# Optimization experiments

Hardware: AMD Instinct MI355X
Metric: run time of the kernel (lower is better)

The kernel has to match this reference:

```python
import math
import jax, jax.numpy as jnp
import numpy as np

B, N = 1, 512
C_S, C_Z, C_H, H, PQ, PV = 384, 128, 16, 12, 4, 8
CONCAT = H * C_Z + H * C_H + H * PV * 3 + H * PV  # 2112
W_C = math.sqrt(2.0 / (9.0 * PQ))
W_L = math.sqrt(1.0 / 3.0)


def setup_inputs() -> dict:
    key = jax.random.key(0)
    ks = jax.random.split(key, 16)
    sc = 0.02
    return {
        "s": jax.random.normal(ks[0], (B, N, C_S), jnp.float32),
        "z": jax.random.normal(ks[1], (B, N, N, C_Z), jnp.float32),
        "R": jax.random.normal(ks[2], (B, N, 3, 3), jnp.float32),
        "t": jax.random.normal(ks[3], (B, N, 3), jnp.float32),
        "mask": jnp.ones((B, N), dtype=bool),
        "Wqkv": jax.random.normal(ks[4], (C_S, 3 * H * C_H), jnp.float32) * sc,
        "Wqk_pts": jax.random.normal(ks[5], (C_S, 2 * H * PQ * 3), jnp.float32) * sc,
        "bqk_pts": jnp.zeros((2 * H * PQ * 3,), jnp.float32),
        "Wv_pts": jax.random.normal(ks[6], (C_S, H * PV * 3), jnp.float32) * sc,
        "bv_pts": jnp.zeros((H * PV * 3,), jnp.float32),
        "Wb": jax.random.normal(ks[7], (C_Z, H), jnp.float32) * sc,
        "bb": jnp.zeros((H,), jnp.float32),
        "gamma": jnp.full((H,), 0.541324854612918, jnp.float32),
        "Wfin": jax.random.normal(ks[8], (CONCAT, C_S), jnp.float32) * sc,
        "bfin": jnp.zeros((C_S,), jnp.float32),
    }


def _apply_rigid(R, t, pts):
    # R: [B,N,3,3], t: [B,N,3], pts: [B,N,H,P,3] -> global frame
    return jnp.einsum('bnxy,bnhpy->bnhpx', R, pts) + t[:, :, None, None, :]


def _invert_apply_rigid(R, t, pts):
    # R^T (pts - t)
    return jnp.einsum('bnyx,bnhpy->bnhpx', R, pts - t[:, :, None, None, :])


def reference(s, z, R, t, mask, Wqkv, Wqk_pts, bqk_pts, Wv_pts, bv_pts,
              Wb, bb, gamma, Wfin, bfin):
    b_, n_ = s.shape[0], s.shape[1]
    qkv = (s @ Wqkv).reshape(b_, n_, 3, H, C_H)
    q, k, v = qkv[:, :, 0], qkv[:, :, 1], qkv[:, :, 2]
    term1 = jnp.einsum('bihc,bjhc->bhij', q, k) / math.sqrt(C_H)
    term2 = jnp.transpose(z @ Wb + bb, (0, 3, 1, 2))  # [B,H,i,j]

    qk_pts = (s @ Wqk_pts + bqk_pts).reshape(b_, n_, 2, H, PQ, 3)
    q_pts, k_pts = qk_pts[:, :, 0], qk_pts[:, :, 1]
    qg = _apply_rigid(R, t, q_pts)  # [B,N,H,PQ,3]
    kg = _apply_rigid(R, t, k_pts)
    # squared distance summed over points and xyz -> [B,i,j,H]
    diff2 = jnp.sum((qg[:, :, None] - kg[:, None]) ** 2, axis=(-2, -1))
    term3 = (jax.nn.softplus(gamma)[None, :, None, None] * (W_C / 2.0)
             * jnp.transpose(diff2, (0, 3, 1, 2)))

    logits = W_L * (term1 + term2 - term3)
    logits = jnp.where(mask[:, None, None, :], logits, -1e9)
    aw = jax.nn.softmax(logits, axis=-1)  # [B,H,i,j]

    out_tilde = jnp.einsum('bhij,bijc->bihc', aw, z)
    out = jnp.einsum('bhij,bjhc->bihc', aw, v)

    v_pts = (s @ Wv_pts + bv_pts).reshape(b_, n_, H, PV, 3)
    vg = _apply_rigid(R, t, v_pts)
    o_global = jnp.einsum('bhij,bjhvx->bihvx', aw, vg)
    o_vec = _invert_apply_rigid(R, t, o_global)  # [B,N,H,PV,3]
    o_norm = jnp.sqrt(jnp.sum(o_vec ** 2, axis=-1) + 1e-8)

    feats = jnp.concatenate([
        out_tilde.reshape(b_, n_, -1),
        out.reshape(b_, n_, -1),
        o_vec.reshape(b_, n_, -1),
        o_norm.reshape(b_, n_, -1),
    ], axis=-1)
    return feats @ Wfin + bfin
```

## Files before the change

### kernel.cpp

```cpp
#include <hip/hip_runtime.h>
#include <math.h>

#define NSEQ 512
#define CS   384
#define NH   12
#define CHD  16
#define CZ   128
#define CONCATD 2112

#define W_L      0.57735026918962576f
#define W_C_HALF 0.117851130197757925f

typedef float f32x4 __attribute__((ext_vector_type(4)));
typedef short bf16x8 __attribute__((ext_vector_type(8)));
typedef unsigned int u32x2 __attribute__((ext_vector_type(2)));
typedef unsigned int u32x4 __attribute__((ext_vector_type(4)));

__device__ __forceinline__ unsigned short f2bf(float f) {
    union { float f; unsigned int u; } v; v.f = f;
    unsigned int u = v.u + 0x7FFFu + ((v.u >> 16) & 1u);
    return (unsigned short)(u >> 16);
}
__device__ __forceinline__ float bf2f(unsigned short u) {
    union { unsigned int i; float f; } v; v.i = ((unsigned int)u) << 16; return v.f;
}

#define MFMA16(A, B, C) __builtin_amdgcn_mfma_f32_16x16x32_bf16((A), (B), (C), 0, 0, 0)

#define RAWBAR() do {                                          \
    __builtin_amdgcn_sched_barrier(0);                         \
    asm volatile("s_waitcnt lgkmcnt(0)" ::: "memory");         \
    __builtin_amdgcn_s_barrier();                              \
    __builtin_amdgcn_sched_barrier(0);                         \
} while (0)

__global__ __launch_bounds__(256) void ipa_prep(
    const float* __restrict__ s, const float* __restrict__ Wqkv,
    const float* __restrict__ Wqk, const float* __restrict__ Wv,
    const float* __restrict__ bqk, const float* __restrict__ bv,
    const float* __restrict__ Wfin,
    unsigned short* __restrict__ sb, unsigned short* __restrict__ WcatT,
    float* __restrict__ biasv, unsigned short* __restrict__ WfinT)
{
    __shared__ float tile[32][33];
    if (blockIdx.x >= 314) {
        int b = blockIdx.x - 314;
        int kt = b / 12, nt = b - kt * 12;
        int k0 = kt * 32, n0 = nt * 32;
        #pragma unroll
        for (int it = 0; it < 4; ++it) {
            int idx = it * 256 + threadIdx.x;
            int ty = idx >> 5, tx = idx & 31;
            tile[ty][tx] = Wfin[(size_t)(k0 + ty) * 384 + n0 + tx];
        }
        __syncthreads();
        #pragma unroll
        for (int it = 0; it < 4; ++it) {
            int idx = it * 256 + threadIdx.x;
            int ty = idx >> 5, tx = idx & 31;
            WfinT[(size_t)(n0 + ty) * 2112 + k0 + tx] = f2bf(tile[tx][ty]);
        }
        return;
    }
    int v = blockIdx.x * 256 + threadIdx.x;
    if (v < 24576) {
        const float* src = s + (size_t)v * 8;
        f32x4 a = *(const f32x4*)src, b = *(const f32x4*)(src + 4);
        u32x4 pk;
        pk[0] = (unsigned)f2bf(a[0]) | ((unsigned)f2bf(a[1]) << 16);
        pk[1] = (unsigned)f2bf(a[2]) | ((unsigned)f2bf(a[3]) << 16);
        pk[2] = (unsigned)f2bf(b[0]) | ((unsigned)f2bf(b[1]) << 16);
        pk[3] = (unsigned)f2bf(b[2]) | ((unsigned)f2bf(b[3]) << 16);
        *(u32x4*)(sb + (size_t)v * 8) = pk;
    } else if (v < 79872) {
        int v2 = v - 24576;
        int n = v2 / 48;
        int kq = (v2 - n * 48) * 8;
        const float* W; int stride; int col; float sc = 1.f;
        if (n < 576)      { W = Wqkv; stride = 576; col = n;       if (n < 192) sc = 0.25f; }
        else if (n < 864) { W = Wqk;  stride = 288; col = n - 576; }
        else              { W = Wv;   stride = 288; col = n - 864; }
        const float* src = W + (size_t)kq * stride + col;
        unsigned int pk[4];
        #pragma unroll
        for (int e = 0; e < 4; ++e) {
            float v0 = src[(size_t)(2 * e) * stride] * sc;
            float v1 = src[(size_t)(2 * e + 1) * stride] * sc;
            pk[e] = (unsigned)f2bf(v0) | ((unsigned)f2bf(v1) << 16);
        }
        u32x4 pkv = {pk[0], pk[1], pk[2], pk[3]};
        *(u32x4*)(WcatT + (size_t)n * 384 + kq) = pkv;
    } else if (v < 80160) {
        int c0 = (v - 79872) * 4;
        #pragma unroll
        for (int e = 0; e < 4; ++e) {
            int c = c0 + e;
            biasv[c] = (c < 576) ? 0.f : ((c < 864) ? bqk[c - 576] : bv[c - 864]);
        }
    }
}

__global__ __launch_bounds__(128) void ipa_projgemm(
    const unsigned short* __restrict__ sb, const unsigned short* __restrict__ WcatT,
    const float* __restrict__ biasv, float* __restrict__ proj)
{
    const int n0 = blockIdx.x * 64, m0 = blockIdx.y * 32;
    const int tid = threadIdx.x, lane = tid & 63, wv = tid >> 6;
    __shared__ __align__(16) unsigned short A_l[32][136];
    __shared__ __align__(16) unsigned short B_l[64][136];
    f32x4 C[4];
    const f32x4 ZV = {0.f, 0.f, 0.f, 0.f};
    #pragma unroll
    for (int nf = 0; nf < 4; ++nf) C[nf] = ZV;

    #pragma unroll
    for (int kc = 0; kc < 3; ++kc) {
        const int k0 = kc * 128;
        __syncthreads();
        #pragma unroll
        for (int it = 0; it < 4; ++it) {
            int v = it * 128 + tid;
            int row = v >> 4, c8 = v & 15;
            *(u32x4*)&A_l[row][c8 * 8] =
                *(const u32x4*)(sb + (size_t)(m0 + row) * 384 + k0 + c8 * 8);
        }
        #pragma unroll
        for (int it = 0; it < 8; ++it) {
            int v = it * 128 + tid;
            int row = v >> 4, c8 = v & 15;
            *(u32x4*)&B_l[row][c8 * 8] =
                *(const u32x4*)(WcatT + (size_t)(n0 + row) * 384 + k0 + c8 * 8);
        }
        __syncthreads();
        const int koff = (lane >> 4) * 8;
        #pragma unroll
        for (int ks = 0; ks < 4; ++ks) {
            bf16x8 Af = *(const bf16x8*)&A_l[wv * 16 + (lane & 15)][ks * 32 + koff];
            #pragma unroll
            for (int nf = 0; nf < 4; ++nf) {
                bf16x8 Bf = *(const bf16x8*)&B_l[nf * 16 + (lane & 15)][ks * 32 + koff];
                C[nf] = MFMA16(Af, Bf, C[nf]);
            }
        }
    }
    #pragma unroll
    for (int nf = 0; nf < 4; ++nf) {
        int col = n0 + nf * 16 + (lane & 15);
        float bval = biasv[col];
        #pragma unroll
        for (int r = 0; r < 4; ++r) {
            int row = m0 + wv * 16 + (lane >> 4) * 4 + r;
            proj[(size_t)row * 1152 + col] = C[nf][r] + bval;
        }
    }
}

__global__ __launch_bounds__(256) void ipa_projep(
    const float* __restrict__ proj, const float* __restrict__ R, const float* __restrict__ t,
    const float* __restrict__ gamma,
    unsigned short* __restrict__ Aaug, unsigned short* __restrict__ Baug,
    unsigned short* __restrict__ VcatT, float* __restrict__ rq, float* __restrict__ rk)
{
    const int half = threadIdx.x >> 7;
    const int i = blockIdx.x * 2 + half;
    const int st = threadIdx.x & 127;
    __shared__ float R_l[2][9], t_l[2][3], sq_l[2][96];
    __shared__ float sh_l[12];

    if (st < 9) R_l[half][st] = R[i * 9 + st];
    if (st >= 12 && st < 15) t_l[half][st - 12] = t[i * 3 + st - 12];
    if (threadIdx.x >= 240 && threadIdx.x < 252) {
        int h = threadIdx.x - 240;
        float spg = logf(1.f + __expf(gamma[h])) * W_C_HALF;
        sh_l[h] = sqrtf(2.f * spg);
    }
    __syncthreads();

    const float* row = proj + (size_t)i * 1152;

    for (int c = st; c < 576; c += 128) {
        unsigned short b16 = f2bf(row[c]);
        if (c < 192) {
            Aaug[((size_t)(c >> 4) * 512 + i) * 32 + (c & 15)] = b16;
        } else if (c < 384) {
            int cc = c - 192;
            Baug[((size_t)(cc >> 4) * 512 + i) * 32 + (cc & 15)] = b16;
        } else {
            int cc = c - 384;
            VcatT[((size_t)((cc >> 4) * 48 + (cc & 15))) * 512 + i] = b16;
        }
    }

    const float* Rr = R_l[half];
    const float* tt = t_l[half];
    for (int pt = st; pt < 192; pt += 128) {
        if (pt < 96) {
            int lp = (pt < 48) ? pt : pt - 48;
            int h = lp >> 2, p = lp & 3;
            int base = 576 + pt * 3;
            float p0 = row[base], p1 = row[base + 1], p2 = row[base + 2];
            float sh = sh_l[h];
            float g0 = (Rr[0] * p0 + Rr[1] * p1 + Rr[2] * p2 + tt[0]) * sh;
            float g1 = (Rr[3] * p0 + Rr[4] * p1 + Rr[5] * p2 + tt[1]) * sh;
            float g2 = (Rr[6] * p0 + Rr[7] * p1 + Rr[8] * p2 + tt[2]) * sh;
            sq_l[half][pt] = g0 * g0 + g1 * g1 + g2 * g2;
            unsigned short* dst =
                (pt < 48 ? Aaug : Baug) + ((size_t)h * 512 + i) * 32 + 16 + p * 3;
            dst[0] = f2bf(g0); dst[1] = f2bf(g1); dst[2] = f2bf(g2);
        } else {
            int vp = pt - 96;
            int h = vp >> 3, vv = vp & 7;
            int base = 864 + vp * 3;
            float p0 = row[base], p1 = row[base + 1], p2 = row[base + 2];
            float g0 = Rr[0] * p0 + Rr[1] * p1 + Rr[2] * p2 + tt[0];
            float g1 = Rr[3] * p0 + Rr[4] * p1 + Rr[5] * p2 + tt[1];
            float g2 = Rr[6] * p0 + Rr[7] * p1 + Rr[8] * p2 + tt[2];
            size_t rbase = ((size_t)h * 48 + 16 + vv * 3) * 512 + i;
            VcatT[rbase] = f2bf(g0);
            VcatT[rbase + 512] = f2bf(g1);
            VcatT[rbase + 1024] = f2bf(g2);
        }
    }
    __syncthreads();

    if (st < 24) {
        int qk = st / 12, h = st - qk * 12;
        int b0 = qk * 48 + h * 4;
        float ssum = sq_l[half][b0] + sq_l[half][b0 + 1]
                   + sq_l[half][b0 + 2] + sq_l[half][b0 + 3];
        (qk ? rk : rq)[h * 512 + i] = 0.5f * ssum;
    }
    if (st >= 32 && st < 56) {
        int e = st - 32;
        int mt = e / 12, h = e - mt * 12;
        *(unsigned long long*)((mt ? Baug : Aaug) + ((size_t)h * 512 + i) * 32 + 28) = 0ull;
    }
}

__global__ __launch_bounds__(256) void ipa_term2n(
    const float* __restrict__ z, const float* __restrict__ Wb, const float* __restrict__ bb,
    unsigned short* __restrict__ S)
{
    const int i = blockIdx.x >> 3;
    const int j0 = (blockIdx.x & 7) * 64;
    const int tid = threadIdx.x, lane = tid & 63, wv = tid >> 6;
    const int l15 = lane & 15, hi = lane >> 4;
    const int koff = hi * 8;
    __shared__ __align__(16) unsigned short z_l[64][136];

    bf16x8 wbf[4];
    #pragma unroll
    for (int ks = 0; ks < 4; ++ks) {
        bf16x8 rfr;
        #pragma unroll
        for (int e = 0; e < 8; ++e) {
            int c = ks * 32 + koff + e;
            float w = (l15 < 12) ? Wb[c * 12 + l15] : 0.f;
            rfr[e] = (short)f2bf(w);
        }
        wbf[ks] = rfr;
    }
    float bbv[4];
    #pragma unroll
    for (int r = 0; r < 4; ++r) { int h = hi * 4 + r; bbv[r] = (h < 12) ? bb[h] : 0.f; }

    #pragma unroll
    for (int it = 0; it < 4; ++it) {
        int u = it * 256 + tid;
        int row = u >> 4, c8 = u & 15;
        const float* src = z + ((size_t)(i * 512 + j0 + row)) * 128 + c8 * 8;
        f32x4 a = *(const f32x4*)src, b = *(const f32x4*)(src + 4);
        u32x4 pk;
        pk[0] = (unsigned)f2bf(a[0]) | ((unsigned)f2bf(a[1]) << 16);
        pk[1] = (unsigned)f2bf(a[2]) | ((unsigned)f2bf(a[3]) << 16);
        pk[2] = (unsigned)f2bf(b[0]) | ((unsigned)f2bf(b[1]) << 16);
        pk[3] = (unsigned)f2bf(b[2]) | ((unsigned)f2bf(b[3]) << 16);
        *(u32x4*)&z_l[row][c8 * 8] = pk;
    }
    __syncthreads();

    const int jcol = wv * 16 + l15;
    f32x4 C = {0.f, 0.f, 0.f, 0.f};
    #pragma unroll
    for (int ks = 0; ks < 4; ++ks)
        C = MFMA16(wbf[ks], *(const bf16x8*)&z_l[jcol][ks * 32 + koff], C);
    #pragma unroll
    for (int r = 0; r < 4; ++r) {
        int h = hi * 4 + r;
        if (h < 12)
            S[(size_t)h * 262144 + (size_t)i * 512 + j0 + jcol] = f2bf(C[r] + bbv[r]);
    }
}

__global__ __launch_bounds__(256) void ipa_smax(
    const unsigned short* __restrict__ S, const unsigned short* __restrict__ Aaug,
    const unsigned short* __restrict__ Baug, const float* __restrict__ rq,
    const float* __restrict__ rk, unsigned short* __restrict__ P1, float* __restrict__ l1)
{
    const int h = blockIdx.x, i0 = blockIdx.y * 16;
    const int tid = threadIdx.x, lane = tid & 63, wv = tid >> 6;
    const int col = lane & 15, hi = lane >> 4;
    __shared__ __align__(16) unsigned short Baug_l[512][40];
    __shared__ __align__(16) unsigned short Aaug_l[16][40];
    __shared__ float rk_l[512], rq_l[16];
    __shared__ float pmx[4][16], psm[4][16];

    for (int u = tid; u < 2048; u += 256) {
        int row = u >> 2, seg = u & 3;
        *(u32x4*)&Baug_l[row][seg * 8] =
            *(const u32x4*)(Baug + ((size_t)h * 512 + row) * 32 + seg * 8);
    }
    if (tid < 64) {
        int row = tid >> 2, seg = tid & 3;
        *(u32x4*)&Aaug_l[row][seg * 8] =
            *(const u32x4*)(Aaug + ((size_t)h * 512 + i0 + row) * 32 + seg * 8);
    }
    for (int u = tid; u < 512; u += 256) rk_l[u] = rk[h * 512 + u];
    if (tid >= 64 && tid < 80) rq_l[tid - 64] = rq[h * 512 + i0 + tid - 64];
    __syncthreads();

    const f32x4 ZV = {0.f, 0.f, 0.f, 0.f};
    bf16x8 Af = *(const bf16x8*)&Aaug_l[col][hi * 8];
    f32x4 C[8];
    #pragma unroll
    for (int nf = 0; nf < 8; ++nf) {
        int n = wv * 8 + nf;
        bf16x8 Bf = *(const bf16x8*)&Baug_l[n * 16 + col][hi * 8];
        C[nf] = MFMA16(Af, Bf, ZV);
    }
    const unsigned short* Srow = S + (size_t)h * 262144 + (size_t)i0 * 512;
    float rmax[4] = {-1e30f, -1e30f, -1e30f, -1e30f};
    #pragma unroll
    for (int nf = 0; nf < 8; ++nf) {
        int j = wv * 128 + nf * 16 + col;
        float rkj = rk_l[j];
        #pragma unroll
        for (int r = 0; r < 4; ++r) {
            int il = hi * 4 + r;
            float Sv = bf2f(Srow[(size_t)il * 512 + j]);
            float L = W_L * (C[nf][r] + Sv - rq_l[il] - rkj);
            C[nf][r] = L;
            rmax[r] = fmaxf(rmax[r], L);
        }
    }
    #pragma unroll
    for (int o = 8; o; o >>= 1)
        #pragma unroll
        for (int r = 0; r < 4; ++r) rmax[r] = fmaxf(rmax[r], __shfl_xor(rmax[r], o));
    if (col == 0)
        #pragma unroll
        for (int r = 0; r < 4; ++r) pmx[wv][hi * 4 + r] = rmax[r];
    __syncthreads();
    float M[4], lsum[4] = {0.f, 0.f, 0.f, 0.f};
    #pragma unroll
    for (int r = 0; r < 4; ++r) {
        int il = hi * 4 + r;
        M[r] = fmaxf(fmaxf(pmx[0][il], pmx[1][il]), fmaxf(pmx[2][il], pmx[3][il]));
    }
    #pragma unroll
    for (int nf = 0; nf < 8; ++nf)
        #pragma unroll
        for (int r = 0; r < 4; ++r) {
            float p = __expf(C[nf][r] - M[r]);
            C[nf][r] = p;
            lsum[r] += p;
        }
    #pragma unroll
    for (int o = 8; o; o >>= 1)
        #pragma unroll
        for (int r = 0; r < 4; ++r) lsum[r] += __shfl_xor(lsum[r], o);
    if (col == 0)
        #pragma unroll
        for (int r = 0; r < 4; ++r) psm[wv][hi * 4 + r] = lsum[r];
    __syncthreads();
    if (wv == 0 && col == 0) {
        #pragma unroll
        for (int r = 0; r < 4; ++r) {
            int il = hi * 4 + r;
            l1[h * 512 + i0 + il] = psm[0][il] + psm[1][il] + psm[2][il] + psm[3][il];
        }
    }
    unsigned short* Prow = P1 + (size_t)h * 262144 + (size_t)i0 * 512;
    #pragma unroll
    for (int nf = 0; nf < 8; ++nf) {
        int j = wv * 128 + nf * 16 + col;
        #pragma unroll
        for (int r = 0; r < 4; ++r)
            Prow[(size_t)(hi * 4 + r) * 512 + j] = f2bf(C[nf][r]);
    }
}

__global__ __launch_bounds__(256) void ipa_ot2(
    const float* __restrict__ z, const unsigned short* __restrict__ P1,
    const float* __restrict__ l1, unsigned short* __restrict__ featsb)
{
    const int bid = blockIdx.x;
    const int i = bid >> 1;
    const int chalf = (bid & 1) * 64;
    const int tid = threadIdx.x, lane = tid & 63, wv = tid >> 6;
    const int l15 = lane & 15, hi = lane >> 4;
    const int koff = hi * 8;
    __shared__ __align__(16) unsigned short P_l[16][520];
    __shared__ __align__(16) unsigned short zT[2][64][72];

    for (int u = tid; u < 1024; u += 256) {
        int row = u >> 6, c8 = u & 63;
        *(u32x4*)&P_l[row][c8 * 8] =
            *(const u32x4*)(P1 + (size_t)row * 262144 + (size_t)i * 512 + c8 * 8);
    }
    __syncthreads();

    f32x4 sa[4];
    #pragma unroll
    for (int it = 0; it < 4; ++it) {
        int u = it * 256 + tid;
        int jj = u >> 4, c4l = u & 15;
        sa[it] = *(const f32x4*)(z + ((size_t)(i * 512 + jj)) * 128 + chalf + c4l * 4);
    }

    const f32x4 ZV = {0.f, 0.f, 0.f, 0.f};
    f32x4 Co = ZV;

    for (int jt = 0; jt < 8; ++jt) {
        const int cur = jt & 1;
        #pragma unroll
        for (int it = 0; it < 4; ++it) {
            int u = it * 256 + tid;
            int jj = u >> 4, c4l = u & 15;
            f32x4 zv = sa[it];
            unsigned short b0 = f2bf(zv[0]), b1 = f2bf(zv[1]), b2 = f2bf(zv[2]), b3 = f2bf(zv[3]);
            unsigned int w01 = (unsigned)b0 | ((unsigned)b1 << 16);
            unsigned int w23 = (unsigned)b2 | ((unsigned)b3 << 16);
            unsigned int p01 = (unsigned int)__shfl_xor((int)w01, 16);
            unsigned int p23 = (unsigned int)__shfl_xor((int)w23, 16);
            bool even = ((tid & 16) == 0);
            unsigned short q0 = (unsigned short)(p01 & 0xffff), q1 = (unsigned short)(p01 >> 16);
            unsigned short q2 = (unsigned short)(p23 & 0xffff), q3 = (unsigned short)(p23 >> 16);
            unsigned int w0, w1, w2, w3;
            if (even) {
                w0 = (unsigned)b0 | ((unsigned)q0 << 16); w1 = (unsigned)b1 | ((unsigned)q1 << 16);
                w2 = (unsigned)b2 | ((unsigned)q2 << 16); w3 = (unsigned)b3 | ((unsigned)q3 << 16);
            } else {
                w0 = (unsigned)q0 | ((unsigned)b0 << 16); w1 = (unsigned)q1 | ((unsigned)b1 << 16);
                w2 = (unsigned)q2 | ((unsigned)b2 << 16); w3 = (unsigned)q3 | ((unsigned)b3 << 16);
            }
            int jp = jj >> 1;
            int rot = ((c4l >> 1) & 3) + (even ? 0 : 2);
            #pragma unroll
            for (int ss = 0; ss < 2; ++ss) {
                int rr = (rot + ss) & 3;
                unsigned int val = (rr == 0) ? w0 : ((rr == 1) ? w1 : ((rr == 2) ? w2 : w3));
                *(unsigned int*)&zT[cur][4 * c4l + rr][2 * jp] = val;
            }
        }
        if (jt < 7) {
            const int j0n = (jt + 1) * 64;
            #pragma unroll
            for (int it = 0; it < 4; ++it) {
                int u = it * 256 + tid;
                int jj = u >> 4, c4l = u & 15;
                sa[it] = *(const f32x4*)(z + ((size_t)(i * 512 + j0n + jj)) * 128 + chalf + c4l * 4);
            }
        }
        RAWBAR();
        #pragma unroll
        for (int ks2 = 0; ks2 < 2; ++ks2) {
            bf16x8 Af = *(const bf16x8*)&P_l[l15][jt * 64 + ks2 * 32 + koff];
            bf16x8 Bf = *(const bf16x8*)&zT[cur][wv * 16 + l15][ks2 * 32 + koff];
            Co = MFMA16(Af, Bf, Co);
        }
    }

    #pragma unroll
    for (int r = 0; r < 4; ++r) {
        int h = hi * 4 + r;
        if (h < 12)
            featsb[(size_t)i * CONCATD + h * 128 + chalf + wv * 16 + l15]
                = f2bf(Co[r] / l1[h * 512 + i]);
    }
}

__global__ __launch_bounds__(256) void ipa_pv(
    const unsigned short* __restrict__ P1, const unsigned short* __restrict__ VcatT,
    const float* __restrict__ l1, const float* __restrict__ R,
    const float* __restrict__ t, unsigned short* __restrict__ featsb)
{
    const int h = blockIdx.x, i0 = blockIdx.y * 64;
    const int tid = threadIdx.x, lane = tid & 63, wv = tid >> 6;
    const int col = lane & 15, hi = lane >> 4;
    __shared__ __align__(16) unsigned short V_l[48][520];
    __shared__ float ogl[64][26];

    for (int u = tid; u < 3072; u += 256) {
        int row = u >> 6, c8 = u & 63;
        *(u32x4*)&V_l[row][c8 * 8] =
            *(const u32x4*)(VcatT + ((size_t)h * 48 + row) * 512 + c8 * 8);
    }
    __syncthreads();
    f32x4 C0 = {0.f,0.f,0.f,0.f}, C1 = C0, C2 = C0;
    const unsigned short* Pbase =
        P1 + (size_t)h * 262144 + (size_t)(i0 + wv * 16 + col) * 512;
    #pragma unroll
    for (int ks = 0; ks < 16; ++ks) {
        bf16x8 Af = *(const bf16x8*)(Pbase + ks * 32 + hi * 8);
        C0 = MFMA16(Af, *(const bf16x8*)&V_l[col][ks * 32 + hi * 8],      C0);
        C1 = MFMA16(Af, *(const bf16x8*)&V_l[16 + col][ks * 32 + hi * 8], C1);
        C2 = MFMA16(Af, *(const bf16x8*)&V_l[32 + col][ks * 32 + hi * 8], C2);
    }
    #pragma unroll
    for (int r = 0; r < 4; ++r) {
        int il = wv * 16 + hi * 4 + r;
        int irow = i0 + il;
        float inv = 1.f / l1[h * 512 + irow];
        featsb[(size_t)irow * CONCATD + 1536 + h * 16 + col] = f2bf(C0[r] * inv);
        ogl[il][col] = C1[r] * inv;
        if (col < 8) ogl[il][16 + col] = C2[r] * inv;
    }
    __syncthreads();

    #pragma unroll
    for (int it = 0; it < 2; ++it) {
        int item = it * 256 + tid;
        int il = item >> 3, v = item & 7;
        int i = i0 + il;
        const float* Rr = R + i * 9;
        const float* tt = t + i * 3;
        float g0 = ogl[il][v * 3 + 0] - tt[0];
        float g1 = ogl[il][v * 3 + 1] - tt[1];
        float g2 = ogl[il][v * 3 + 2] - tt[2];
        float o0 = Rr[0] * g0 + Rr[3] * g1 + Rr[6] * g2;
        float o1 = Rr[1] * g0 + Rr[4] * g1 + Rr[7] * g2;
        float o2 = Rr[2] * g0 + Rr[5] * g1 + Rr[8] * g2;
        unsigned short* frow = featsb + (size_t)i * CONCATD;
        frow[1728 + h * 24 + v * 3 + 0] = f2bf(o0);
        frow[1728 + h * 24 + v * 3 + 1] = f2bf(o1);
        frow[1728 + h * 24 + v * 3 + 2] = f2bf(o2);
        frow[2016 + h * 8 + v] = f2bf(sqrtf(o0 * o0 + o1 * o1 + o2 * o2 + 1e-8f));
    }
}

__global__ __launch_bounds__(128) void ipa_finalb(
    const unsigned short* __restrict__ featsb, const unsigned short* __restrict__ WfinT,
    float* __restrict__ fpart)
{
    const int n0 = blockIdx.x * 64, m0 = blockIdx.y * 32;
    const int k0 = blockIdx.z * 192;
    const int tid = threadIdx.x, lane = tid & 63, wv = tid >> 6;
    const int l15 = lane & 15, hi = lane >> 4;
    __shared__ __align__(16) unsigned short A_l[32][200];
    __shared__ __align__(16) unsigned short B_l[64][200];

    #pragma unroll
    for (int it = 0; it < 6; ++it) {
        int v = it * 128 + tid;
        int row = v / 24, c8 = v % 24;
        *(u32x4*)&A_l[row][c8 * 8] =
            *(const u32x4*)(featsb + (size_t)(m0 + row) * CONCATD + k0 + c8 * 8);
    }
    #pragma unroll
    for (int it = 0; it < 12; ++it) {
        int v = it * 128 + tid;
        int row = v / 24, c8 = v % 24;
        *(u32x4*)&B_l[row][c8 * 8] =
            *(const u32x4*)(WfinT + (size_t)(n0 + row) * 2112 + k0 + c8 * 8);
    }
    __syncthreads();

    const f32x4 ZV = {0.f, 0.f, 0.f, 0.f};
    f32x4 C[4];
    #pragma unroll
    for (int nf = 0; nf < 4; ++nf) C[nf] = ZV;
    const int koff = hi * 8;
    #pragma unroll
    for (int ks = 0; ks < 6; ++ks) {
        bf16x8 Af = *(const bf16x8*)&A_l[wv * 16 + l15][ks * 32 + koff];
        #pragma unroll
        for (int nf = 0; nf < 4; ++nf) {
            bf16x8 Bf = *(const bf16x8*)&B_l[nf * 16 + l15][ks * 32 + koff];
            C[nf] = MFMA16(Af, Bf, C[nf]);
        }
    }
    float* P = fpart + (size_t)blockIdx.z * (NSEQ * CS);
    #pragma unroll
    for (int nf = 0; nf < 4; ++nf) {
        int colx = n0 + nf * 16 + l15;
        #pragma unroll
        for (int r = 0; r < 4; ++r) {
            int row = m0 + wv * 16 + hi * 4 + r;
            P[(size_t)row * CS + colx] = C[nf][r];
        }
    }
}

__global__ __launch_bounds__(256) void ipa_reduceb(
    const float* __restrict__ fpart, const float* __restrict__ bias, float* __restrict__ out)
{
    int idx = blockIdx.x * 256 + threadIdx.x;
    f32x4 acc = ((const f32x4*)bias)[idx % (CS / 4)];
    #pragma unroll
    for (int kc = 0; kc < 11; ++kc)
        acc += ((const f32x4*)(fpart + (size_t)kc * (NSEQ * CS)))[idx];
    ((f32x4*)out)[idx] = acc;
}

extern "C" void kernel_launch(void* const* d_in, const int* in_sizes, int n_in,
                              void* d_out, int out_size, void* d_ws, size_t ws_size,
                              hipStream_t stream) {
    (void)in_sizes; (void)n_in; (void)out_size; (void)ws_size;
    const float* s    = (const float*)d_in[0];
    const float* z    = (const float*)d_in[1];
    const float* R    = (const float*)d_in[2];
    const float* t    = (const float*)d_in[3];
    const float* Wqkv = (const float*)d_in[5];
    const float* Wqk  = (const float*)d_in[6];
    const float* bqk  = (const float*)d_in[7];
    const float* Wv   = (const float*)d_in[8];
    const float* bv   = (const float*)d_in[9];
    const float* Wb   = (const float*)d_in[10];
    const float* bb   = (const float*)d_in[11];
    const float* gam  = (const float*)d_in[12];
    const float* Wfin = (const float*)d_in[13];
    const float* bfin = (const float*)d_in[14];
    float* out = (float*)d_out;

    char* w8 = (char*)d_ws;
    unsigned short* S     = (unsigned short*)(w8 + 0);
    unsigned short* P1    = (unsigned short*)(w8 + 6291456);
    unsigned short* featsb= (unsigned short*)(w8 + 12582912);
    unsigned short* WfinT = (unsigned short*)(w8 + 14745600);
    unsigned short* Aaug  = (unsigned short*)(w8 + 16908288);
    unsigned short* Baug  = (unsigned short*)(w8 + 17301504);
    unsigned short* VcatT = (unsigned short*)(w8 + 17694720);
    float* rq             = (float*)(w8 + 18284544);
    float* rk             = (float*)(w8 + 18309120);
    float* l1             = (float*)(w8 + 18333696);
    float* fpart          = (float*)(w8 + 0);
    float* proj           = (float*)(w8 + 0);
    unsigned short* sb    = (unsigned short*)(w8 + 2359296);
    unsigned short* WcatT = (unsigned short*)(w8 + 2752512);
    float* biasv          = (float*)(w8 + 3637248);

    ipa_prep<<<1106, 256, 0, stream>>>(s, Wqkv, Wqk, Wv, bqk, bv, Wfin,
                                       sb, WcatT, biasv, WfinT);
    ipa_projgemm<<<dim3(18, 16), 128, 0, stream>>>(sb, WcatT, biasv, proj);
    ipa_projep<<<256, 256, 0, stream>>>(proj, R, t, gam, Aaug, Baug, VcatT, rq, rk);
    ipa_term2n<<<4096, 256, 0, stream>>>(z, Wb, bb, S);
    ipa_smax<<<dim3(12, 32), 256, 0, stream>>>(S, Aaug, Baug, rq, rk, P1, l1);
    ipa_ot2<<<1024, 256, 0, stream>>>(z, P1, l1, featsb);
    ipa_pv<<<dim3(12, 8), 256, 0, stream>>>(P1, VcatT, l1, R, t, featsb);
    ipa_finalb<<<dim3(6, 16, 11), 128, 0, stream>>>(featsb, WfinT, fpart);
    ipa_reduceb<<<192, 256, 0, stream>>>(fpart, bfin, out);
}
```

Measured before the change: 93.33 us.

## Merge independent kernels into heterogeneous launches to cut launch count

Combines the projection GEMM with the z·Wb pair-bias kernel into one launch that branches on block index, and combines the out_tilde and point-value attention kernels likewise. Workspace buffers are relocated so the merged kernels do not overwrite each other's data. The intent is to remove launch gaps and let small, low-occupancy kernels overlap with larger ones. In exchange, the projection blocks leave half their warps idle, the PV path now stages V in two halves, and shared-memory sizing is set by the larger branch.

```diff
diff --git a/kernel.cpp b/kernel.cpp
--- a/kernel.cpp
+++ b/kernel.cpp
@@ -100,57 +100,117 @@
     }
 }
 
-__global__ __launch_bounds__(128) void ipa_projgemm(
+__global__ __launch_bounds__(256) void ipa_pg_t2(
     const unsigned short* __restrict__ sb, const unsigned short* __restrict__ WcatT,
-    const float* __restrict__ biasv, float* __restrict__ proj)
+    const float* __restrict__ biasv, float* __restrict__ proj,
+    const float* __restrict__ z, const float* __restrict__ Wb,
+    const float* __restrict__ bb, unsigned short* __restrict__ S)
 {
-    const int n0 = blockIdx.x * 64, m0 = blockIdx.y * 32;
+    __shared__ __align__(16) char smem[26112];
     const int tid = threadIdx.x, lane = tid & 63, wv = tid >> 6;
-    __shared__ __align__(16) unsigned short A_l[32][136];
-    __shared__ __align__(16) unsigned short B_l[64][136];
-    f32x4 C[4];
+    const int l15 = lane & 15, hi = lane >> 4;
+    const int koff = hi * 8;
     const f32x4 ZV = {0.f, 0.f, 0.f, 0.f};
-    #pragma unroll
-    for (int nf = 0; nf < 4; ++nf) C[nf] = ZV;
-
-    #pragma unroll
-    for (int kc = 0; kc < 3; ++kc) {
-        const int k0 = kc * 128;
-        __syncthreads();
-        #pragma unroll
-        for (int it = 0; it < 4; ++it) {
-            int v = it * 128 + tid;
-            int row = v >> 4, c8 = v & 15;
-            *(u32x4*)&A_l[row][c8 * 8] =
-                *(const u32x4*)(sb + (size_t)(m0 + row) * 384 + k0 + c8 * 8);
-        }
-        #pragma unroll
-        for (int it = 0; it < 8; ++it) {
-            int v = it * 128 + tid;
-            int row = v >> 4, c8 = v & 15;
-            *(u32x4*)&B_l[row][c8 * 8] =
-                *(const u32x4*)(WcatT + (size_t)(n0 + row) * 384 + k0 + c8 * 8);
-        }
-        __syncthreads();
-        const int koff = (lane >> 4) * 8;
-        #pragma unroll
-        for (int ks = 0; ks < 4; ++ks) {
-            bf16x8 Af = *(const bf16x8*)&A_l[wv * 16 + (lane & 15)][ks * 32 + koff];
+
+    if (blockIdx.x < 288) {
+        const int n0 = ((int)blockIdx.x % 18) * 64;
+        const int m0 = ((int)blockIdx.x / 18) * 32;
+        unsigned short (*A_l)[136] = (unsigned short(*)[136])smem;
+        unsigned short (*B_l)[136] = (unsigned short(*)[136])(smem + 8704);
+        f32x4 C[4];
+        #pragma unroll
+        for (int nf = 0; nf < 4; ++nf) C[nf] = ZV;
+
+        #pragma unroll
+        for (int kc = 0; kc < 3; ++kc) {
+            const int k0 = kc * 128;
+            __syncthreads();
+            #pragma unroll
+            for (int it = 0; it < 2; ++it) {
+                int v = it * 256 + tid;
+                int row = v >> 4, c8 = v & 15;
+                *(u32x4*)&A_l[row][c8 * 8] =
+                    *(const u32x4*)(sb + (size_t)(m0 + row) * 384 + k0 + c8 * 8);
+            }
+            #pragma unroll
+            for (int it = 0; it < 4; ++it) {
+                int v = it * 256 + tid;
+                int row = v >> 4, c8 = v & 15;
+                *(u32x4*)&B_l[row][c8 * 8] =
+                    *(const u32x4*)(WcatT + (size_t)(n0 + row) * 384 + k0 + c8 * 8);
+            }
+            __syncthreads();
+            if (wv < 2) {
+                #pragma unroll
+                for (int ks = 0; ks < 4; ++ks) {
+                    bf16x8 Af = *(const bf16x8*)&A_l[wv * 16 + l15][ks * 32 + koff];
+                    #pragma unroll
+                    for (int nf = 0; nf < 4; ++nf) {
+                        bf16x8 Bf = *(const bf16x8*)&B_l[nf * 16 + l15][ks * 32 + koff];
+                        C[nf] = MFMA16(Af, Bf, C[nf]);
+                    }
+                }
+            }
+        }
+        if (wv < 2) {
             #pragma unroll
             for (int nf = 0; nf < 4; ++nf) {
-                bf16x8 Bf = *(const bf16x8*)&B_l[nf * 16 + (lane & 15)][ks * 32 + koff];
-                C[nf] = MFMA16(Af, Bf, C[nf]);
-            }
-        }
-    }
-    #pragma unroll
-    for (int nf = 0; nf < 4; ++nf) {
-        int col = n0 + nf * 16 + (lane & 15);
-        float bval = biasv[col];
+                int col = n0 + nf * 16 + l15;
+                float bval = biasv[col];
+                #pragma unroll
+                for (int r = 0; r < 4; ++r) {
+                    int row = m0 + wv * 16 + hi * 4 + r;
+                    proj[(size_t)row * 1152 + col] = C[nf][r] + bval;
+                }
+            }
+        }
+    } else {
+        const int b = blockIdx.x - 288;
+        const int i = b >> 3;
+        const int j0 = (b & 7) * 64;
+        unsigned short (*z_l)[136] = (unsigned short(*)[136])smem;
+
+        bf16x8 wbf[4];
+        #pragma unroll
+        for (int ks = 0; ks < 4; ++ks) {
+            bf16x8 rfr;
+            #pragma unroll
+            for (int e = 0; e < 8; ++e) {
+                int c = ks * 32 + koff + e;
+                float w = (l15 < 12) ? Wb[c * 12 + l15] : 0.f;
+                rfr[e] = (short)f2bf(w);
+            }
+            wbf[ks] = rfr;
+        }
+        float bbv[4];
+        #pragma unroll
+        for (int r = 0; r < 4; ++r) { int h = hi * 4 + r; bbv[r] = (h < 12) ? bb[h] : 0.f; }
+
+        #pragma unroll
+        for (int it = 0; it < 4; ++it) {
+            int u = it * 256 + tid;
+            int row = u >> 4, c8 = u & 15;
+            const float* src = z + ((size_t)(i * 512 + j0 + row)) * 128 + c8 * 8;
+            f32x4 a = *(const f32x4*)src, bq = *(const f32x4*)(src + 4);
+            u32x4 pk;
+            pk[0] = (unsigned)f2bf(a[0]) | ((unsigned)f2bf(a[1]) << 16);
+            pk[1] = (unsigned)f2bf(a[2]) | ((unsigned)f2bf(a[3]) << 16);
+            pk[2] = (unsigned)f2bf(bq[0]) | ((unsigned)f2bf(bq[1]) << 16);
+            pk[3] = (unsigned)f2bf(bq[2]) | ((unsigned)f2bf(bq[3]) << 16);
+            *(u32x4*)&z_l[row][c8 * 8] = pk;
+        }
+        __syncthreads();
+
+        const int jcol = wv * 16 + l15;
+        f32x4 C = ZV;
+        #pragma unroll
+        for (int ks = 0; ks < 4; ++ks)
+            C = MFMA16(wbf[ks], *(const bf16x8*)&z_l[jcol][ks * 32 + koff], C);
         #pragma unroll
         for (int r = 0; r < 4; ++r) {
-            int row = m0 + wv * 16 + (lane >> 4) * 4 + r;
-            proj[(size_t)row * 1152 + col] = C[nf][r] + bval;
+            int h = hi * 4 + r;
+            if (h < 12)
+                S[(size_t)h * 262144 + (size_t)i * 512 + j0 + jcol] = f2bf(C[r] + bbv[r]);
         }
     }
 }
@@ -237,61 +297,6 @@
     }
 }
 
-__global__ __launch_bounds__(256) void ipa_term2n(
-    const float* __restrict__ z, const float* __restrict__ Wb, const float* __restrict__ bb,
-    unsigned short* __restrict__ S)
-{
-    const int i = blockIdx.x >> 3;
-    const int j0 = (blockIdx.x & 7) * 64;
-    const int tid = threadIdx.x, lane = tid & 63, wv = tid >> 6;
-    const int l15 = lane & 15, hi = lane >> 4;
-    const int koff = hi * 8;
-    __shared__ __align__(16) unsigned short z_l[64][136];
-
-    bf16x8 wbf[4];
-    #pragma unroll
-    for (int ks = 0; ks < 4; ++ks) {
-        bf16x8 rfr;
-        #pragma unroll
-        for (int e = 0; e < 8; ++e) {
-            int c = ks * 32 + koff + e;
-            float w = (l15 < 12) ? Wb[c * 12 + l15] : 0.f;
-            rfr[e] = (short)f2bf(w);
-        }
-        wbf[ks] = rfr;
-    }
-    float bbv[4];
-    #pragma unroll
-    for (int r = 0; r < 4; ++r) { int h = hi * 4 + r; bbv[r] = (h < 12) ? bb[h] : 0.f; }
-
-    #pragma unroll
-    for (int it = 0; it < 4; ++it) {
-        int u = it * 256 + tid;
-        int row = u >> 4, c8 = u & 15;
-        const float* src = z + ((size_t)(i * 512 + j0 + row)) * 128 + c8 * 8;
-        f32x4 a = *(const f32x4*)src, b = *(const f32x4*)(src + 4);
-        u32x4 pk;
-        pk[0] = (unsigned)f2bf(a[0]) | ((unsigned)f2bf(a[1]) << 16);
-        pk[1] = (unsigned)f2bf(a[2]) | ((unsigned)f2bf(a[3]) << 16);
-        pk[2] = (unsigned)f2bf(b[0]) | ((unsigned)f2bf(b[1]) << 16);
-        pk[3] = (unsigned)f2bf(b[2]) | ((unsigned)f2bf(b[3]) << 16);
-        *(u32x4*)&z_l[row][c8 * 8] = pk;
-    }
-    __syncthreads();
-
-    const int jcol = wv * 16 + l15;
-    f32x4 C = {0.f, 0.f, 0.f, 0.f};
-    #pragma unroll
-    for (int ks = 0; ks < 4; ++ks)
-        C = MFMA16(wbf[ks], *(const bf16x8*)&z_l[jcol][ks * 32 + koff], C);
-    #pragma unroll
-    for (int r = 0; r < 4; ++r) {
-        int h = hi * 4 + r;
-        if (h < 12)
-            S[(size_t)h * 262144 + (size_t)i * 512 + j0 + jcol] = f2bf(C[r] + bbv[r]);
-    }
-}
-
 __global__ __launch_bounds__(256) void ipa_smax(
     const unsigned short* __restrict__ S, const unsigned short* __restrict__ Aaug,
     const unsigned short* __restrict__ Baug, const float* __restrict__ rq,
@@ -390,152 +395,155 @@
     }
 }
 
-__global__ __launch_bounds__(256) void ipa_ot2(
+__global__ __launch_bounds__(256) void ipa_otpv(
     const float* __restrict__ z, const unsigned short* __restrict__ P1,
-    const float* __restrict__ l1, unsigned short* __restrict__ featsb)
+    const float* __restrict__ l1, const unsigned short* __restrict__ VcatT,
+    const float* __restrict__ R, const float* __restrict__ t,
+    unsigned short* __restrict__ featsb)
 {
-    const int bid = blockIdx.x;
-    const int i = bid >> 1;
-    const int chalf = (bid & 1) * 64;
+    __shared__ __align__(16) char smem[35072];
     const int tid = threadIdx.x, lane = tid & 63, wv = tid >> 6;
     const int l15 = lane & 15, hi = lane >> 4;
     const int koff = hi * 8;
-    __shared__ __align__(16) unsigned short P_l[16][520];
-    __shared__ __align__(16) unsigned short zT[2][64][72];
-
-    for (int u = tid; u < 1024; u += 256) {
-        int row = u >> 6, c8 = u & 63;
-        *(u32x4*)&P_l[row][c8 * 8] =
-            *(const u32x4*)(P1 + (size_t)row * 262144 + (size_t)i * 512 + c8 * 8);
-    }
-    __syncthreads();
-
-    f32x4 sa[4];
-    #pragma unroll
-    for (int it = 0; it < 4; ++it) {
-        int u = it * 256 + tid;
-        int jj = u >> 4, c4l = u & 15;
-        sa[it] = *(const f32x4*)(z + ((size_t)(i * 512 + jj)) * 128 + chalf + c4l * 4);
-    }
-
     const f32x4 ZV = {0.f, 0.f, 0.f, 0.f};
-    f32x4 Co = ZV;
-
-    for (int jt = 0; jt < 8; ++jt) {
-        const int cur = jt & 1;
+
+    if (blockIdx.x < 1024) {
+        const int i = blockIdx.x >> 1;
+        const int chalf = ((int)blockIdx.x & 1) * 64;
+        unsigned short (*P_l)[520] = (unsigned short(*)[520])smem;
+        typedef unsigned short zt_t[64][72];
+        zt_t* zT = (zt_t*)(smem + 16640);
+
+        for (int u = tid; u < 1024; u += 256) {
+            int row = u >> 6, c8 = u & 63;
+            *(u32x4*)&P_l[row][c8 * 8] =
+                *(const u32x4*)(P1 + (size_t)row * 262144 + (size_t)i * 512 + c8 * 8);
+        }
+        __syncthreads();
+
+        f32x4 sa[4];
         #pragma unroll
         for (int it = 0; it < 4; ++it) {
             int u = it * 256 + tid;
             int jj = u >> 4, c4l = u & 15;
-            f32x4 zv = sa[it];
-            unsigned short b0 = f2bf(zv[0]), b1 = f2bf(zv[1]), b2 = f2bf(zv[2]), b3 = f2bf(zv[3]);
-            unsigned int w01 = (unsigned)b0 | ((unsigned)b1 << 16);
-            unsigned int w23 = (unsigned)b2 | ((unsigned)b3 << 16);
-            unsigned int p01 = (unsigned int)__shfl_xor((int)w01, 16);
-            unsigned int p23 = (unsigned int)__shfl_xor((int)w23, 16);
-            bool even = ((tid & 16) == 0);
-            unsigned short q0 = (unsigned short)(p01 & 0xffff), q1 = (unsigned short)(p01 >> 16);
-            unsigned short q2 = (unsigned short)(p23 & 0xffff), q3 = (unsigned short)(p23 >> 16);
-            unsigned int w0, w1, w2, w3;
-            if (even) {
-                w0 = (unsigned)b0 | ((unsigned)q0 << 16); w1 = (unsigned)b1 | ((unsigned)q1 << 16);
-                w2 = (unsigned)b2 | ((unsigned)q2 << 16); w3 = (unsigned)b3 | ((unsigned)q3 << 16);
-            } else {
-                w0 = (unsigned)q0 | ((unsigned)b0 << 16); w1 = (unsigned)q1 | ((unsigned)b1 << 16);
-                w2 = (unsigned)q2 | ((unsigned)b2 << 16); w3 = (unsigned)q3 | ((unsigned)b3 << 16);
-            }
-            int jp = jj >> 1;
-            int rot = ((c4l >> 1) & 3) + (even ? 0 : 2);
-            #pragma unroll
-            for (int ss = 0; ss < 2; ++ss) {
-                int rr = (rot + ss) & 3;
-                unsigned int val = (rr == 0) ? w0 : ((rr == 1) ? w1 : ((rr == 2) ? w2 : w3));
-                *(unsigned int*)&zT[cur][4 * c4l + rr][2 * jp] = val;
-            }
-        }
-        if (jt < 7) {
-            const int j0n = (jt + 1) * 64;
+            sa[it] = *(const f32x4*)(z + ((size_t)(i * 512 + jj)) * 128 + chalf + c4l * 4);
+        }
+
+        f32x4 Co = ZV;
+        for (int jt = 0; jt < 8; ++jt) {
+            const int cur = jt & 1;
             #pragma unroll
             for (int it = 0; it < 4; ++it) {
                 int u = it * 256 + tid;
                 int jj = u >> 4, c4l = u & 15;
-                sa[it] = *(const f32x4*)(z + ((size_t)(i * 512 + j0n + jj)) * 128 + chalf + c4l * 4);
-            }
-        }
-        RAWBAR();
-        #pragma unroll
-        for (int ks2 = 0; ks2 < 2; ++ks2) {
-            bf16x8 Af = *(const bf16x8*)&P_l[l15][jt * 64 + ks2 * 32 + koff];
-            bf16x8 Bf = *(const bf16x8*)&zT[cur][wv * 16 + l15][ks2 * 32 + koff];
-            Co = MFMA16(Af, Bf, Co);
-        }
-    }
-
-    #pragma unroll
-    for (int r = 0; r < 4; ++r) {
-        int h = hi * 4 + r;
-        if (h < 12)
-            featsb[(size_t)i * CONCATD + h * 128 + chalf + wv * 16 + l15]
-                = f2bf(Co[r] / l1[h * 512 + i]);
-    }
-}
-
-__global__ __launch_bounds__(256) void ipa_pv(
-    const unsigned short* __restrict__ P1, const unsigned short* __restrict__ VcatT,
-    const float* __restrict__ l1, const float* __restrict__ R,
-    const float* __restrict__ t, unsigned short* __restrict__ featsb)
-{
-    const int h = blockIdx.x, i0 = blockIdx.y * 64;
-    const int tid = threadIdx.x, lane = tid & 63, wv = tid >> 6;
-    const int col = lane & 15, hi = lane >> 4;
-    __shared__ __align__(16) unsigned short V_l[48][520];
-    __shared__ float ogl[64][26];
-
-    for (int u = tid; u < 3072; u += 256) {
-        int row = u >> 6, c8 = u & 63;
-        *(u32x4*)&V_l[row][c8 * 8] =
-            *(const u32x4*)(VcatT + ((size_t)h * 48 + row) * 512 + c8 * 8);
-    }
-    __syncthreads();
-    f32x4 C0 = {0.f,0.f,0.f,0.f}, C1 = C0, C2 = C0;
-    const unsigned short* Pbase =
-        P1 + (size_t)h * 262144 + (size_t)(i0 + wv * 16 + col) * 512;
-    #pragma unroll
-    for (int ks = 0; ks < 16; ++ks) {
-        bf16x8 Af = *(const bf16x8*)(Pbase + ks * 32 + hi * 8);
-        C0 = MFMA16(Af, *(const bf16x8*)&V_l[col][ks * 32 + hi * 8],      C0);
-        C1 = MFMA16(Af, *(const bf16x8*)&V_l[16 + col][ks * 32 + hi * 8], C1);
-        C2 = MFMA16(Af, *(const bf16x8*)&V_l[32 + col][ks * 32 + hi * 8], C2);
-    }
-    #pragma unroll
-    for (int r = 0; r < 4; ++r) {
-        int il = wv * 16 + hi * 4 + r;
-        int irow = i0 + il;
-        float inv = 1.f / l1[h * 512 + irow];
-        featsb[(size_t)irow * CONCATD + 1536 + h * 16 + col] = f2bf(C0[r] * inv);
-        ogl[il][col] = C1[r] * inv;
-        if (col < 8) ogl[il][16 + col] = C2[r] * inv;
-    }
-    __syncthreads();
-
-    #pragma unroll
-    for (int it = 0; it < 2; ++it) {
-        int item = it * 256 + tid;
-        int il = item >> 3, v = item & 7;
-        int i = i0 + il;
-        const float* Rr = R + i * 9;
-        const float* tt = t + i * 3;
-        float g0 = ogl[il][v * 3 + 0] - tt[0];
-        float g1 = ogl[il][v * 3 + 1] - tt[1];
-        float g2 = ogl[il][v * 3 + 2] - tt[2];
-        float o0 = Rr[0] * g0 + Rr[3] * g1 + Rr[6] * g2;
-        float o1 = Rr[1] * g0 + Rr[4] * g1 + Rr[7] * g2;
-        float o2 = Rr[2] * g0 + Rr[5] * g1 + Rr[8] * g2;
-        unsigned short* frow = featsb + (size_t)i * CONCATD;
-        frow[1728 + h * 24 + v * 3 + 0] = f2bf(o0);
-        frow[1728 + h * 24 + v * 3 + 1] = f2bf(o1);
-        frow[1728 + h * 24 + v * 3 + 2] = f2bf(o2);
-        frow[2016 + h * 8 + v] = f2bf(sqrtf(o0 * o0 + o1 * o1 + o2 * o2 + 1e-8f));
+                f32x4 zv = sa[it];
+                unsigned short b0 = f2bf(zv[0]), b1 = f2bf(zv[1]), b2 = f2bf(zv[2]), b3 = f2bf(zv[3]);
+                unsigned int w01 = (unsigned)b0 | ((unsigned)b1 << 16);
+                unsigned int w23 = (unsigned)b2 | ((unsigned)b3 << 16);
+                unsigned int p01 = (unsigned int)__shfl_xor((int)w01, 16);
+                unsigned int p23 = (unsigned int)__shfl_xor((int)w23, 16);
+                bool even = ((tid & 16) == 0);
+                unsigned short q0 = (unsigned short)(p01 & 0xffff), q1 = (unsigned short)(p01 >> 16);
+                unsigned short q2 = (unsigned short)(p23 & 0xffff), q3 = (unsigned short)(p23 >> 16);
+                unsigned int w0, w1, w2, w3;
+                if (even) {
+                    w0 = (unsigned)b0 | ((unsigned)q0 << 16); w1 = (unsigned)b1 | ((unsigned)q1 << 16);
+                    w2 = (unsigned)b2 | ((unsigned)q2 << 16); w3 = (unsigned)b3 | ((unsigned)q3 << 16);
+                } else {
+                    w0 = (unsigned)q0 | ((unsigned)b0 << 16); w1 = (unsigned)q1 | ((unsigned)b1 << 16);
+                    w2 = (unsigned)q2 | ((unsigned)b2 << 16); w3 = (unsigned)q3 | ((unsigned)b3 << 16);
+                }
+                int jp = jj >> 1;
+                int rot = ((c4l >> 1) & 3) + (even ? 0 : 2);
+                #pragma unroll
+                for (int ss = 0; ss < 2; ++ss) {
+                    int rr = (rot + ss) & 3;
+                    unsigned int val = (rr == 0) ? w0 : ((rr == 1) ? w1 : ((rr == 2) ? w2 : w3));
+                    *(unsigned int*)&zT[cur][4 * c4l + rr][2 * jp] = val;
+                }
+            }
+            if (jt < 7) {
+                const int j0n = (jt + 1) * 64;
+                #pragma unroll
+                for (int it = 0; it < 4; ++it) {
+                    int u = it * 256 + tid;
+                    int jj = u >> 4, c4l = u & 15;
+                    sa[it] = *(const f32x4*)(z + ((size_t)(i * 512 + j0n + jj)) * 128 + chalf + c4l * 4);
+                }
+            }
+            RAWBAR();
+            #pragma unroll
+            for (int ks2 = 0; ks2 < 2; ++ks2) {
+                bf16x8 Af = *(const bf16x8*)&P_l[l15][jt * 64 + ks2 * 32 + koff];
+                bf16x8 Bf = *(const bf16x8*)&zT[cur][wv * 16 + l15][ks2 * 32 + koff];
+                Co = MFMA16(Af, Bf, Co);
+            }
+        }
+
+        #pragma unroll
+        for (int r = 0; r < 4; ++r) {
+            int h = hi * 4 + r;
+            if (h < 12)
+                featsb[(size_t)i * CONCATD + h * 128 + chalf + wv * 16 + l15]
+                    = f2bf(Co[r] / l1[h * 512 + i]);
+        }
+    } else {
+        const int b = blockIdx.x - 1024;
+        const int h = b >> 3, i0 = (b & 7) * 64;
+        const int col = l15;
+        unsigned short (*V_l)[264] = (unsigned short(*)[264])smem;
+        float (*ogl)[26] = (float(*)[26])(smem + 25344);
+
+        f32x4 C0 = ZV, C1 = ZV, C2 = ZV;
+        const unsigned short* Pbase =
+            P1 + (size_t)h * 262144 + (size_t)(i0 + wv * 16 + col) * 512;
+        #pragma unroll
+        for (int hf = 0; hf < 2; ++hf) {
+            __syncthreads();
+            for (int u = tid; u < 1536; u += 256) {
+                int row = u >> 5, c8 = u & 31;
+                *(u32x4*)&V_l[row][c8 * 8] =
+                    *(const u32x4*)(VcatT + ((size_t)h * 48 + row) * 512 + hf * 256 + c8 * 8);
+            }
+            __syncthreads();
+            #pragma unroll
+            for (int ks2 = 0; ks2 < 8; ++ks2) {
+                bf16x8 Af = *(const bf16x8*)(Pbase + hf * 256 + ks2 * 32 + hi * 8);
+                C0 = MFMA16(Af, *(const bf16x8*)&V_l[col][ks2 * 32 + hi * 8],      C0);
+                C1 = MFMA16(Af, *(const bf16x8*)&V_l[16 + col][ks2 * 32 + hi * 8], C1);
+                C2 = MFMA16(Af, *(const bf16x8*)&V_l[32 + col][ks2 * 32 + hi * 8], C2);
+            }
+        }
+        #pragma unroll
+        for (int r = 0; r < 4; ++r) {
+            int il = wv * 16 + hi * 4 + r;
+            int irow = i0 + il;
+            float inv = 1.f / l1[h * 512 + irow];
+            featsb[(size_t)irow * CONCATD + 1536 + h * 16 + col] = f2bf(C0[r] * inv);
+            ogl[il][col] = C1[r] * inv;
+            if (col < 8) ogl[il][16 + col] = C2[r] * inv;
+        }
+        __syncthreads();
+
+        #pragma unroll
+        for (int it = 0; it < 2; ++it) {
+            int item = it * 256 + tid;
+            int il = item >> 3, v = item & 7;
+            int i = i0 + il;
+            const float* Rr = R + i * 9;
+            const float* tt = t + i * 3;
+            float g0 = ogl[il][v * 3 + 0] - tt[0];
+            float g1 = ogl[il][v * 3 + 1] - tt[1];
+            float g2 = ogl[il][v * 3 + 2] - tt[2];
+            float o0 = Rr[0] * g0 + Rr[3] * g1 + Rr[6] * g2;
+            float o1 = Rr[1] * g0 + Rr[4] * g1 + Rr[7] * g2;
+            float o2 = Rr[2] * g0 + Rr[5] * g1 + Rr[8] * g2;
+            unsigned short* frow = featsb + (size_t)i * CONCATD;
+            frow[1728 + h * 24 + v * 3 + 0] = f2bf(o0);
+            frow[1728 + h * 24 + v * 3 + 1] = f2bf(o1);
+            frow[1728 + h * 24 + v * 3 + 2] = f2bf(o2);
+            frow[2016 + h * 8 + v] = f2bf(sqrtf(o0 * o0 + o1 * o1 + o2 * o2 + 1e-8f));
+        }
     }
 }
 
@@ -635,19 +643,21 @@
     float* rk             = (float*)(w8 + 18309120);
     float* l1             = (float*)(w8 + 18333696);
     float* fpart          = (float*)(w8 + 0);
-    float* proj           = (float*)(w8 + 0);
+    float* proj           = (float*)(w8 + 6291456 + 2359296);
     unsigned short* sb    = (unsigned short*)(w8 + 2359296);
     unsigned short* WcatT = (unsigned short*)(w8 + 2752512);
     float* biasv          = (float*)(w8 + 3637248);
 
+    sb    = (unsigned short*)(w8 + 12582912);
+    WcatT = (unsigned short*)(w8 + 12582912 + 393216);
+    biasv = (float*)(w8 + 12582912 + 1277952);
+
     ipa_prep<<<1106, 256, 0, stream>>>(s, Wqkv, Wqk, Wv, bqk, bv, Wfin,
                                        sb, WcatT, biasv, WfinT);
-    ipa_projgemm<<<dim3(18, 16), 128, 0, stream>>>(sb, WcatT, biasv, proj);
+    ipa_pg_t2<<<4384, 256, 0, stream>>>(sb, WcatT, biasv, proj, z, Wb, bb, S);
     ipa_projep<<<256, 256, 0, stream>>>(proj, R, t, gam, Aaug, Baug, VcatT, rq, rk);
-    ipa_term2n<<<4096, 256, 0, stream>>>(z, Wb, bb, S);
     ipa_smax<<<dim3(12, 32), 256, 0, stream>>>(S, Aaug, Baug, rq, rk, P1, l1);
-    ipa_ot2<<<1024, 256, 0, stream>>>(z, P1, l1, featsb);
-    ipa_pv<<<dim3(12, 8), 256, 0, stream>>>(P1, VcatT, l1, R, t, featsb);
+    ipa_otpv<<<1120, 256, 0, stream>>>(z, P1, l1, VcatT, R, t, featsb);
     ipa_finalb<<<dim3(6, 16, 11), 128, 0, stream>>>(featsb, WfinT, fpart);
     ipa_reduceb<<<192, 256, 0, stream>>>(fpart, bfin, out);
 }
```

New measurement: 84.84 us. 9.1% less time.
